# Kernel tuning notes

Measured on AMD Instinct MI355X. Metric: run time of the kernel, lower is better.

Reference implementation:

```python
import jax, jax.numpy as jnp
import numpy as np
from jax import lax

DIM = 64


def _dwconv(x, w, b):
    # x: [B,C,H,W], w: [C,1,kh,kw] depthwise, 'same' padding
    kh, kw = w.shape[2], w.shape[3]
    y = lax.conv_general_dilated(
        x, w, window_strides=(1, 1),
        padding=[(kh // 2, kh // 2), (kw // 2, kw // 2)],
        dimension_numbers=("NCHW", "OIHW", "NCHW"),
        feature_group_count=x.shape[1])
    return y + b[None, :, None, None]


def _conv1x1(x, w, b):
    y = lax.conv_general_dilated(
        x, w, window_strides=(1, 1), padding="VALID",
        dimension_numbers=("NCHW", "OIHW", "NCHW"))
    return y + b[None, :, None, None]


def _avgpool3(x):
    # PyTorch AvgPool2d(3,1,1) default count_include_pad=True -> sum/9
    s = lax.reduce_window(x, 0.0, lax.add, (1, 1, 3, 3), (1, 1, 1, 1),
                          [(0, 0), (0, 0), (1, 1), (1, 1)])
    return s / 9.0


def _maxpool3(x):
    return lax.reduce_window(x, -jnp.inf, lax.max, (1, 1, 3, 3), (1, 1, 1, 1),
                             [(0, 0), (0, 0), (1, 1), (1, 1)])


def setup_inputs() -> dict:
    key = jax.random.key(0)
    ks = jax.random.split(key, 18)
    C = DIM
    def w(k, shape):
        fan_in = shape[1] * shape[2] * shape[3]
        bound = 1.0 / np.sqrt(fan_in)
        return jax.random.uniform(k, shape, jnp.float32, -bound, bound)
    def b(k, fan_in):
        bound = 1.0 / np.sqrt(fan_in)
        return jax.random.uniform(k, (C,), jnp.float32, -bound, bound)
    return {
        "x": jax.random.normal(ks[0], (16, C, 128, 128), jnp.float32),
        "w55": w(ks[1], (C, 1, 5, 5)), "b55": b(ks[2], 25),
        "w17_0": w(ks[3], (C, 1, 1, 7)), "b17_0": b(ks[4], 7),
        "w17_1": w(ks[5], (C, 1, 7, 1)), "b17_1": b(ks[6], 7),
        "w111_0": w(ks[7], (C, 1, 1, 11)), "b111_0": b(ks[8], 11),
        "w111_1": w(ks[9], (C, 1, 11, 1)), "b111_1": b(ks[10], 11),
        "w211_0": w(ks[11], (C, 1, 1, 21)), "b211_0": b(ks[12], 21),
        "w211_1": w(ks[13], (C, 1, 21, 1)), "b211_1": b(ks[14], 21),
        "w11": w(ks[15], (C, C, 1, 1)), "b11": b(ks[16], C),
    }


def reference(x, w55, b55, w17_0, b17_0, w17_1, b17_1,
              w111_0, b111_0, w111_1, b111_1,
              w211_0, b211_0, w211_1, b211_1, w11, b11):
    def branch(inp):
        c55 = _dwconv(inp, w55, b55)
        c17 = _dwconv(_dwconv(inp, w17_0, b17_0), w17_1, b17_1)
        c111 = _dwconv(_dwconv(inp, w111_0, b111_0), w111_1, b111_1)
        c211 = _dwconv(_dwconv(inp, w211_0, b211_0), w211_1, b211_1)
        return _conv1x1(c55 + c17 + c111 + c211, w11, b11)

    mixer = branch(x)
    mixer_1 = branch(_avgpool3(x))
    mixer_2 = branch(_maxpool3(x))
    return (mixer + mixer_1 + mixer_2) * x
```

## Files before the change

### kernel.cpp

```cpp
#include <hip/hip_runtime.h>
#include <hip/hip_bf16.h>
#include <cstdint>

#define HH 128
#define WW 128
#define CC 64
#define BB 16
#define PLANE (HH*WW)
#define TPSTR 16512

#define XS_STR    52
#define XRAW_STR  60
#define XSTH_H    8736
#define H7_H      11328
#define UNION_F   7072
#define H11_H     14144
#define H21_H     16960
#define SMEM_FLOATS 12232

__device__ __forceinline__ float lo16(unsigned int u) {
  return __uint_as_float(u << 16);
}
__device__ __forceinline__ float hi16(unsigned int u) {
  return __uint_as_float(u & 0xffff0000u);
}

__global__ __launch_bounds__(256, 3) void k_dwsum(
    const float* __restrict__ x, float* __restrict__ T,
    const float* __restrict__ w55, const float* __restrict__ b55,
    const float* __restrict__ w17_0, const float* __restrict__ b17_0,
    const float* __restrict__ w17_1, const float* __restrict__ b17_1,
    const float* __restrict__ w111_0, const float* __restrict__ b111_0,
    const float* __restrict__ w111_1, const float* __restrict__ b111_1,
    const float* __restrict__ w211_0, const float* __restrict__ b211_0,
    const float* __restrict__ w211_1, const float* __restrict__ b211_1) {
  __shared__ float sm[SMEM_FLOATS];
  __hip_bfloat16* hb = (__hip_bfloat16*)sm;

  const int bid = blockIdx.x;
  const int pl = bid >> 3;
  const int t = bid & 7;
  const int tR0 = (t >> 2) * 64;
  const int tC0 = (t & 3) * 32;
  const int ch = pl & (CC - 1);
  const float* xp = x + (size_t)pl * PLANE;
  float* Tp = T + (size_t)pl * TPSTR;
  const int tid = threadIdx.x;

  {
    float* xraw = sm + UNION_F;
    const int base_r = tR0 - 11, base_c = tC0 - 12;
    for (int i = tid; i < 86 * 14; i += 256) {
      int rr = i / 14;
      int jj = i - rr * 14;
      int gr = base_r + rr;
      int gc = base_c + jj * 4;
      float4 v = make_float4(0.f, 0.f, 0.f, 0.f);
      if ((unsigned)gr < 128u && (unsigned)gc < 128u)
        v = *(const float4*)(xp + gr * WW + gc);
      *(float4*)(xraw + rr * XRAW_STR + jj * 4) = v;
    }
  }
  __syncthreads();

  {
    const float* xraw = sm + UNION_F;
    __hip_bfloat16* xsTh = hb + XSTH_H;
    for (int i = tid; i < 28 * 13; i += 256) {
      int rg = i % 28;
      int jj = i / 28;
      int rr0 = rg * 3;
      const float* rp = xraw + rr0 * XRAW_STR + jj * 4;
      float w[5][8];
      #pragma unroll
      for (int k = 0; k < 5; ++k) {
        float4 a = *(const float4*)(rp + k * XRAW_STR);
        float4 b = *(const float4*)(rp + k * XRAW_STR + 4);
        w[k][0] = a.x; w[k][1] = a.y; w[k][2] = a.z; w[k][3] = a.w;
        w[k][4] = b.x; w[k][5] = b.y; w[k][6] = b.z; w[k][7] = b.w;
      }
      int gc0 = tC0 + jj * 4 - 12;
      bool cv[7];
      #pragma unroll
      for (int p = 1; p <= 6; ++p) cv[p] = (unsigned)(gc0 + p) < 128u;

      #pragma unroll
      for (int k = 0; k < 3; ++k) {
        int rr = rr0 + k;
        int gr = tR0 + rr - 10;
        bool rv0 = (unsigned)(gr - 1) < 128u;
        bool rv1 = (unsigned)(gr) < 128u;
        bool rv2 = (unsigned)(gr + 1) < 128u;
        float M0[7], M1[7], M2[7];
        #pragma unroll
        for (int p = 1; p <= 6; ++p) {
          M0[p] = (rv0 && cv[p]) ? w[k][p] : -3.402823466e38f;
          M1[p] = (rv1 && cv[p]) ? w[k + 1][p] : -3.402823466e38f;
          M2[p] = (rv2 && cv[p]) ? w[k + 2][p] : -3.402823466e38f;
        }
        float uq[4];
        #pragma unroll
        for (int q = 0; q < 4; ++q) {
          float s = w[k][q + 1] + w[k][q + 2] + w[k][q + 3] + w[k + 1][q + 1] +
                    w[k + 1][q + 2] + w[k + 1][q + 3] + w[k + 2][q + 1] +
                    w[k + 2][q + 2] + w[k + 2][q + 3];
          float m = fmaxf(
              fmaxf(fmaxf(M0[q + 1], M0[q + 2]), fmaxf(M0[q + 3], M1[q + 1])),
              fmaxf(fmaxf(M1[q + 2], M1[q + 3]),
                    fmaxf(fmaxf(M2[q + 1], M2[q + 2]), M2[q + 3])));
          float val = w[k + 1][q + 2] + s * (1.f / 9.f) + m;
          bool vo = rv1 && ((unsigned)(gc0 + q + 2) < 128u);
          uq[q] = vo ? val : 0.f;
        }
        *(float4*)(sm + rr * XS_STR + jj * 4) =
            make_float4(uq[0], uq[1], uq[2], uq[3]);
        int rt = rr - 8;
        if ((unsigned)rt < 68u) {
          #pragma unroll
          for (int q = 0; q < 4; ++q) {
            int ct = jj * 4 + q - 8;
            if ((unsigned)ct < 36u)
              xsTh[ct * 72 + rt] = __float2bfloat16(uq[q]);
          }
        }
      }
    }
  }

  float k7[7], k11[11], k21[21];
  #pragma unroll
  for (int i = 0; i < 7; ++i) k7[i] = w17_0[ch * 7 + i];
  #pragma unroll
  for (int i = 0; i < 11; ++i) k11[i] = w111_0[ch * 11 + i];
  #pragma unroll
  for (int i = 0; i < 21; ++i) k21[i] = w211_0[ch * 21 + i];
  float bb7 = 3.f * b17_0[ch];
  float bb11 = 3.f * b111_0[ch];
  float bb21 = 3.f * b211_0[ch];

  __syncthreads();

  for (int it = tid; it < 84 * 4; it += 256) {
    int rr = it % 84;
    int cg = it / 84;
    float w[28];
    const float* xr = sm + rr * XS_STR + cg * 8;
    #pragma unroll
    for (int j = 0; j < 7; ++j) {
      float4 v = *(const float4*)(xr + 4 * j);
      w[4 * j] = v.x; w[4 * j + 1] = v.y; w[4 * j + 2] = v.z; w[4 * j + 3] = v.w;
    }
    int gr = tR0 + rr - 10;
    bool rv = (unsigned)gr < 128u;
    bool v11r = (rr >= 5) && (rr <= 78);
    bool v7r = (rr >= 7) && (rr <= 76);
    #pragma unroll
    for (int j = 0; j < 8; ++j) {
      float a21 = bb21, a11 = bb11, a7 = bb7;
      #pragma unroll
      for (int d = 0; d < 21; ++d) a21 += k21[d] * w[j + d];
      #pragma unroll
      for (int d = 0; d < 11; ++d) a11 += k11[d] * w[j + 5 + d];
      #pragma unroll
      for (int d = 0; d < 7; ++d) a7 += k7[d] * w[j + 7 + d];
      int c = cg * 8 + j;
      hb[H21_H + c * 88 + rr] = __float2bfloat16(rv ? a21 : 0.f);
      if (v11r) hb[H11_H + c * 88 + rr - 5] = __float2bfloat16(rv ? a11 : 0.f);
      if (v7r) hb[H7_H + c * 88 + rr - 7] = __float2bfloat16(rv ? a7 : 0.f);
    }
  }

  float v7a[7], v11a[11], v21a[21], w5a[25];
  #pragma unroll
  for (int i = 0; i < 7; ++i) v7a[i] = w17_1[ch * 7 + i];
  #pragma unroll
  for (int i = 0; i < 11; ++i) v11a[i] = w111_1[ch * 11 + i];
  #pragma unroll
  for (int i = 0; i < 21; ++i) v21a[i] = w211_1[ch * 21 + i];
  #pragma unroll
  for (int i = 0; i < 25; ++i) w5a[i] = w55[ch * 25 + i];
  float bsum = 3.f * (b55[ch] + b17_1[ch] + b111_1[ch] + b211_1[ch]);

  __syncthreads();

  {
    int c = tid & 31;
    int r0 = (tid >> 5) * 8;
    float acc[8];
    #pragma unroll
    for (int j = 0; j < 8; ++j) acc[j] = bsum;

    float A[28];
    {
      const unsigned* p = (const unsigned*)&hb[H21_H + c * 88 + r0];
      uint4 q0 = *(const uint4*)p;
      uint4 q1 = *(const uint4*)(p + 4);
      uint4 q2 = *(const uint4*)(p + 8);
      uint2 q3 = *(const uint2*)(p + 12);
      A[0]=lo16(q0.x);A[1]=hi16(q0.x);A[2]=lo16(q0.y);A[3]=hi16(q0.y);
      A[4]=lo16(q0.z);A[5]=hi16(q0.z);A[6]=lo16(q0.w);A[7]=hi16(q0.w);
      A[8]=lo16(q1.x);A[9]=hi16(q1.x);A[10]=lo16(q1.y);A[11]=hi16(q1.y);
      A[12]=lo16(q1.z);A[13]=hi16(q1.z);A[14]=lo16(q1.w);A[15]=hi16(q1.w);
      A[16]=lo16(q2.x);A[17]=hi16(q2.x);A[18]=lo16(q2.y);A[19]=hi16(q2.y);
      A[20]=lo16(q2.z);A[21]=hi16(q2.z);A[22]=lo16(q2.w);A[23]=hi16(q2.w);
      A[24]=lo16(q3.x);A[25]=hi16(q3.x);A[26]=lo16(q3.y);A[27]=hi16(q3.y);
      #pragma unroll
      for (int d = 0; d < 21; ++d)
        #pragma unroll
        for (int j = 0; j < 8; ++j) acc[j] += v21a[d] * A[d + j];
    }
    {
      const unsigned* p = (const unsigned*)&hb[H11_H + c * 88 + r0];
      uint4 q0 = *(const uint4*)p;
      uint4 q1 = *(const uint4*)(p + 4);
      uint2 q2 = *(const uint2*)(p + 8);
      A[0]=lo16(q0.x);A[1]=hi16(q0.x);A[2]=lo16(q0.y);A[3]=hi16(q0.y);
      A[4]=lo16(q0.z);A[5]=hi16(q0.z);A[6]=lo16(q0.w);A[7]=hi16(q0.w);
      A[8]=lo16(q1.x);A[9]=hi16(q1.x);A[10]=lo16(q1.y);A[11]=hi16(q1.y);
      A[12]=lo16(q1.z);A[13]=hi16(q1.z);A[14]=lo16(q1.w);A[15]=hi16(q1.w);
      A[16]=lo16(q2.x);A[17]=hi16(q2.x);
      #pragma unroll
      for (int d = 0; d < 11; ++d)
        #pragma unroll
        for (int j = 0; j < 8; ++j) acc[j] += v11a[d] * A[d + j];
    }
    {
      const unsigned* p = (const unsigned*)&hb[H7_H + c * 88 + r0];
      uint4 q0 = *(const uint4*)p;
      uint4 q1 = *(const uint4*)(p + 4);
      A[0]=lo16(q0.x);A[1]=hi16(q0.x);A[2]=lo16(q0.y);A[3]=hi16(q0.y);
      A[4]=lo16(q0.z);A[5]=hi16(q0.z);A[6]=lo16(q0.w);A[7]=hi16(q0.w);
      A[8]=lo16(q1.x);A[9]=hi16(q1.x);A[10]=lo16(q1.y);A[11]=hi16(q1.y);
      A[12]=lo16(q1.z);A[13]=hi16(q1.z);
      #pragma unroll
      for (int d = 0; d < 7; ++d)
        #pragma unroll
        for (int j = 0; j < 8; ++j) acc[j] += v7a[d] * A[d + j];
    }
    {
      #pragma unroll
      for (int dc = 0; dc < 5; ++dc) {
        const unsigned* p = (const unsigned*)&hb[XSTH_H + (c + dc) * 72 + r0];
        uint4 q0 = *(const uint4*)p;
        uint2 q1 = *(const uint2*)(p + 4);
        float X[12];
        X[0]=lo16(q0.x);X[1]=hi16(q0.x);X[2]=lo16(q0.y);X[3]=hi16(q0.y);
        X[4]=lo16(q0.z);X[5]=hi16(q0.z);X[6]=lo16(q0.w);X[7]=hi16(q0.w);
        X[8]=lo16(q1.x);X[9]=hi16(q1.x);X[10]=lo16(q1.y);X[11]=hi16(q1.y);
        #pragma unroll
        for (int dr = 0; dr < 5; ++dr)
          #pragma unroll
          for (int j = 0; j < 8; ++j) acc[j] += w5a[dr * 5 + dc] * X[j + dr];
      }
    }
    #pragma unroll
    for (int j = 0; j < 8; ++j)
      Tp[(size_t)(tR0 + r0 + j) * WW + tC0 + c] = acc[j];
  }
}

__global__ __launch_bounds__(256, 3) void k_mix(const float* __restrict__ T,
                                                const float* __restrict__ x,
                                                const float* __restrict__ w11,
                                                const float* __restrict__ b11,
                                                float* __restrict__ out) {
  __shared__ float sm[64 * 128 + 64 * 68];
  float* Ts = sm;
  float* Wt = sm + 64 * 128;

  int bid = blockIdx.x;
  int b = bid >> 7;
  int px0 = (bid & 127) * 128;
  int tid = threadIdx.x;

  const float* Tb = T + (size_t)b * 64 * TPSTR + px0;
  for (int i = tid; i < 2048; i += 256) {
    int ci = i >> 5;
    int g = (i & 31) * 4;
    *(float4*)(Ts + ci * 128 + g) =
        *(const float4*)(Tb + (size_t)ci * TPSTR + g);
  }
  for (int i = tid; i < 4096; i += 256) {
    int co = i >> 6, ci = i & 63;
    Wt[ci * 68 + co] = w11[i];
  }
  __syncthreads();

  int pxg = tid & 31;
  int cog = tid >> 5;
  const float* tp = Ts + pxg * 4;
  const float* wp = Wt + cog * 8;

  float acc[8][4];
  #pragma unroll
  for (int a = 0; a < 8; ++a)
    #pragma unroll
    for (int p = 0; p < 4; ++p) acc[a][p] = 0.f;

  #pragma unroll
  for (int k = 0; k < 64; ++k) {
    float4 tv = *(const float4*)(tp + k * 128);
    float4 q0 = *(const float4*)(wp + k * 68);
    float4 q1 = *(const float4*)(wp + k * 68 + 4);
    float wf[8] = {q0.x, q0.y, q0.z, q0.w, q1.x, q1.y, q1.z, q1.w};
    float tvv[4] = {tv.x, tv.y, tv.z, tv.w};
    #pragma unroll
    for (int a = 0; a < 8; ++a)
      #pragma unroll
      for (int p = 0; p < 4; ++p) acc[a][p] += wf[a] * tvv[p];
  }

  const float* xb = x + (size_t)b * (CC * PLANE) + px0 + pxg * 4;
  float* ob = out + (size_t)b * (CC * PLANE) + px0 + pxg * 4;
  #pragma unroll
  for (int a = 0; a < 8; ++a) {
    int co = cog * 8 + a;
    float bb = 3.f * b11[co];
    float4 xv = *(const float4*)(xb + (size_t)co * PLANE);
    float4 o;
    o.x = (acc[a][0] + bb) * xv.x;
    o.y = (acc[a][1] + bb) * xv.y;
    o.z = (acc[a][2] + bb) * xv.z;
    o.w = (acc[a][3] + bb) * xv.w;
    *(float4*)(ob + (size_t)co * PLANE) = o;
  }
}

extern "C" void kernel_launch(void* const* d_in, const int* in_sizes, int n_in,
                              void* d_out, int out_size, void* d_ws,
                              size_t ws_size, hipStream_t stream) {
  const float* x = (const float*)d_in[0];
  const float* w55 = (const float*)d_in[1];
  const float* b55 = (const float*)d_in[2];
  const float* w17_0 = (const float*)d_in[3];
  const float* b17_0 = (const float*)d_in[4];
  const float* w17_1 = (const float*)d_in[5];
  const float* b17_1 = (const float*)d_in[6];
  const float* w111_0 = (const float*)d_in[7];
  const float* b111_0 = (const float*)d_in[8];
  const float* w111_1 = (const float*)d_in[9];
  const float* b111_1 = (const float*)d_in[10];
  const float* w211_0 = (const float*)d_in[11];
  const float* b211_0 = (const float*)d_in[12];
  const float* w211_1 = (const float*)d_in[13];
  const float* b211_1 = (const float*)d_in[14];
  const float* w11 = (const float*)d_in[15];
  const float* b11 = (const float*)d_in[16];
  float* outp = (float*)d_out;

  float* T = (float*)d_ws;

  k_dwsum<<<BB * CC * 8, 256, 0, stream>>>(
      x, T, w55, b55, w17_0, b17_0, w17_1, b17_1, w111_0, b111_0, w111_1,
      b111_1, w211_0, b211_0, w211_1, b211_1);
  k_mix<<<BB * 128, 256, 0, stream>>>(T, x, w11, b11, outp);
}
```

Before: 306.2 us.

## Halve dwsum raw staging buffer and double-buffer mix kernel with direct LDS loads

k_dwsum now loads the input halo tile in two 44-row halves into a smaller raw buffer, running the pool/transpose phase per half. This cuts shared memory so launch bounds can rise to 4 blocks per CU, at the cost of an extra barrier round. k_mix now streams T in 16-channel chunks into a double-buffered LDS tile using global_load_lds, and prefetches x early. Both aim to overlap loads with FMA work and raise occupancy, but they add synchronisation and extra register pressure from holding the x values.

```diff
diff --git a/kernel.cpp b/kernel.cpp
--- a/kernel.cpp
+++ b/kernel.cpp
@@ -16,7 +16,7 @@
 #define UNION_F   7072
 #define H11_H     14144
 #define H21_H     16960
-#define SMEM_FLOATS 12232
+#define SMEM_FLOATS 9888
 
 __device__ __forceinline__ float lo16(unsigned int u) {
   return __uint_as_float(u << 16);
@@ -25,7 +25,72 @@
   return __uint_as_float(u & 0xffff0000u);
 }
 
-__global__ __launch_bounds__(256, 3) void k_dwsum(
+__device__ __forceinline__ void phase_a2_half(
+    float* sm, __hip_bfloat16* hb, const float* xbuf, int tid, int tR0,
+    int tC0, int rg_lo, int roff) {
+  __hip_bfloat16* xsTh = hb + XSTH_H;
+  for (int i = tid; i < 14 * 13; i += 256) {
+    int rg = rg_lo + (i % 14);
+    int jj = i / 14;
+    int rr0 = rg * 3;
+    const float* rp = xbuf + (rr0 - roff) * XRAW_STR + jj * 4;
+    float w[5][8];
+    #pragma unroll
+    for (int k = 0; k < 5; ++k) {
+      float4 a = *(const float4*)(rp + k * XRAW_STR);
+      float4 b = *(const float4*)(rp + k * XRAW_STR + 4);
+      w[k][0] = a.x; w[k][1] = a.y; w[k][2] = a.z; w[k][3] = a.w;
+      w[k][4] = b.x; w[k][5] = b.y; w[k][6] = b.z; w[k][7] = b.w;
+    }
+    int gc0 = tC0 + jj * 4 - 12;
+    bool cv[7];
+    #pragma unroll
+    for (int p = 1; p <= 6; ++p) cv[p] = (unsigned)(gc0 + p) < 128u;
+
+    #pragma unroll
+    for (int k = 0; k < 3; ++k) {
+      int rr = rr0 + k;
+      int gr = tR0 + rr - 10;
+      bool rv0 = (unsigned)(gr - 1) < 128u;
+      bool rv1 = (unsigned)(gr) < 128u;
+      bool rv2 = (unsigned)(gr + 1) < 128u;
+      float M0[7], M1[7], M2[7];
+      #pragma unroll
+      for (int p = 1; p <= 6; ++p) {
+        M0[p] = (rv0 && cv[p]) ? w[k][p] : -3.402823466e38f;
+        M1[p] = (rv1 && cv[p]) ? w[k + 1][p] : -3.402823466e38f;
+        M2[p] = (rv2 && cv[p]) ? w[k + 2][p] : -3.402823466e38f;
+      }
+      float uq[4];
+      #pragma unroll
+      for (int q = 0; q < 4; ++q) {
+        float s = w[k][q + 1] + w[k][q + 2] + w[k][q + 3] + w[k + 1][q + 1] +
+                  w[k + 1][q + 2] + w[k + 1][q + 3] + w[k + 2][q + 1] +
+                  w[k + 2][q + 2] + w[k + 2][q + 3];
+        float m = fmaxf(
+            fmaxf(fmaxf(M0[q + 1], M0[q + 2]), fmaxf(M0[q + 3], M1[q + 1])),
+            fmaxf(fmaxf(M1[q + 2], M1[q + 3]),
+                  fmaxf(fmaxf(M2[q + 1], M2[q + 2]), M2[q + 3])));
+        float val = w[k + 1][q + 2] + s * (1.f / 9.f) + m;
+        bool vo = rv1 && ((unsigned)(gc0 + q + 2) < 128u);
+        uq[q] = vo ? val : 0.f;
+      }
+      *(float4*)(sm + rr * XS_STR + jj * 4) =
+          make_float4(uq[0], uq[1], uq[2], uq[3]);
+      int rt = rr - 8;
+      if ((unsigned)rt < 68u) {
+        #pragma unroll
+        for (int q = 0; q < 4; ++q) {
+          int ct = jj * 4 + q - 8;
+          if ((unsigned)ct < 36u)
+            xsTh[ct * 72 + rt] = __float2bfloat16(uq[q]);
+        }
+      }
+    }
+  }
+}
+
+__global__ __launch_bounds__(256, 4) void k_dwsum(
     const float* __restrict__ x, float* __restrict__ T,
     const float* __restrict__ w55, const float* __restrict__ b55,
     const float* __restrict__ w17_0, const float* __restrict__ b17_0,
@@ -47,85 +112,34 @@
   float* Tp = T + (size_t)pl * TPSTR;
   const int tid = threadIdx.x;
 
-  {
-    float* xraw = sm + UNION_F;
-    const int base_r = tR0 - 11, base_c = tC0 - 12;
-    for (int i = tid; i < 86 * 14; i += 256) {
-      int rr = i / 14;
-      int jj = i - rr * 14;
-      int gr = base_r + rr;
-      int gc = base_c + jj * 4;
-      float4 v = make_float4(0.f, 0.f, 0.f, 0.f);
-      if ((unsigned)gr < 128u && (unsigned)gc < 128u)
-        v = *(const float4*)(xp + gr * WW + gc);
-      *(float4*)(xraw + rr * XRAW_STR + jj * 4) = v;
-    }
-  }
-  __syncthreads();
-
-  {
-    const float* xraw = sm + UNION_F;
-    __hip_bfloat16* xsTh = hb + XSTH_H;
-    for (int i = tid; i < 28 * 13; i += 256) {
-      int rg = i % 28;
-      int jj = i / 28;
-      int rr0 = rg * 3;
-      const float* rp = xraw + rr0 * XRAW_STR + jj * 4;
-      float w[5][8];
-      #pragma unroll
-      for (int k = 0; k < 5; ++k) {
-        float4 a = *(const float4*)(rp + k * XRAW_STR);
-        float4 b = *(const float4*)(rp + k * XRAW_STR + 4);
-        w[k][0] = a.x; w[k][1] = a.y; w[k][2] = a.z; w[k][3] = a.w;
-        w[k][4] = b.x; w[k][5] = b.y; w[k][6] = b.z; w[k][7] = b.w;
-      }
-      int gc0 = tC0 + jj * 4 - 12;
-      bool cv[7];
-      #pragma unroll
-      for (int p = 1; p <= 6; ++p) cv[p] = (unsigned)(gc0 + p) < 128u;
-
-      #pragma unroll
-      for (int k = 0; k < 3; ++k) {
-        int rr = rr0 + k;
-        int gr = tR0 + rr - 10;
-        bool rv0 = (unsigned)(gr - 1) < 128u;
-        bool rv1 = (unsigned)(gr) < 128u;
-        bool rv2 = (unsigned)(gr + 1) < 128u;
-        float M0[7], M1[7], M2[7];
-        #pragma unroll
-        for (int p = 1; p <= 6; ++p) {
-          M0[p] = (rv0 && cv[p]) ? w[k][p] : -3.402823466e38f;
-          M1[p] = (rv1 && cv[p]) ? w[k + 1][p] : -3.402823466e38f;
-          M2[p] = (rv2 && cv[p]) ? w[k + 2][p] : -3.402823466e38f;
-        }
-        float uq[4];
-        #pragma unroll
-        for (int q = 0; q < 4; ++q) {
-          float s = w[k][q + 1] + w[k][q + 2] + w[k][q + 3] + w[k + 1][q + 1] +
-                    w[k + 1][q + 2] + w[k + 1][q + 3] + w[k + 2][q + 1] +
-                    w[k + 2][q + 2] + w[k + 2][q + 3];
-          float m = fmaxf(
-              fmaxf(fmaxf(M0[q + 1], M0[q + 2]), fmaxf(M0[q + 3], M1[q + 1])),
-              fmaxf(fmaxf(M1[q + 2], M1[q + 3]),
-                    fmaxf(fmaxf(M2[q + 1], M2[q + 2]), M2[q + 3])));
-          float val = w[k + 1][q + 2] + s * (1.f / 9.f) + m;
-          bool vo = rv1 && ((unsigned)(gc0 + q + 2) < 128u);
-          uq[q] = vo ? val : 0.f;
-        }
-        *(float4*)(sm + rr * XS_STR + jj * 4) =
-            make_float4(uq[0], uq[1], uq[2], uq[3]);
-        int rt = rr - 8;
-        if ((unsigned)rt < 68u) {
-          #pragma unroll
-          for (int q = 0; q < 4; ++q) {
-            int ct = jj * 4 + q - 8;
-            if ((unsigned)ct < 36u)
-              xsTh[ct * 72 + rt] = __float2bfloat16(uq[q]);
-          }
-        }
-      }
-    }
-  }
+  float* xbuf = sm + UNION_F;
+  const int base_r = tR0 - 11, base_c = tC0 - 12;
+
+  for (int i = tid; i < 44 * 14; i += 256) {
+    int rr = i / 14;
+    int jj = i - rr * 14;
+    int gr = base_r + rr;
+    int gc = base_c + jj * 4;
+    float4 v = make_float4(0.f, 0.f, 0.f, 0.f);
+    if ((unsigned)gr < 128u && (unsigned)gc < 128u)
+      v = *(const float4*)(xp + gr * WW + gc);
+    *(float4*)(xbuf + rr * XRAW_STR + jj * 4) = v;
+  }
+  __syncthreads();
+  phase_a2_half(sm, hb, xbuf, tid, tR0, tC0, 0, 0);
+  __syncthreads();
+  for (int i = tid; i < 44 * 14; i += 256) {
+    int rr = i / 14;
+    int jj = i - rr * 14;
+    int gr = base_r + 42 + rr;
+    int gc = base_c + jj * 4;
+    float4 v = make_float4(0.f, 0.f, 0.f, 0.f);
+    if ((unsigned)gr < 128u && (unsigned)gc < 128u)
+      v = *(const float4*)(xp + gr * WW + gc);
+    *(float4*)(xbuf + rr * XRAW_STR + jj * 4) = v;
+  }
+  __syncthreads();
+  phase_a2_half(sm, hb, xbuf, tid, tR0, tC0, 14, 42);
 
   float k7[7], k11[11], k21[21];
   #pragma unroll
@@ -259,69 +273,92 @@
   }
 }
 
-__global__ __launch_bounds__(256, 3) void k_mix(const float* __restrict__ T,
+__device__ __forceinline__ void gload_lds16(const float* g, float* l) {
+  __builtin_amdgcn_global_load_lds(
+      (const __attribute__((address_space(1))) void*)g,
+      (__attribute__((address_space(3))) void*)l, 16, 0, 0);
+}
+
+__global__ __launch_bounds__(256, 4) void k_mix(const float* __restrict__ T,
                                                 const float* __restrict__ x,
                                                 const float* __restrict__ w11,
                                                 const float* __restrict__ b11,
                                                 float* __restrict__ out) {
-  __shared__ float sm[64 * 128 + 64 * 68];
-  float* Ts = sm;
-  float* Wt = sm + 64 * 128;
+  __shared__ float Tbuf[2][16 * 128];
+  __shared__ float Wt[64 * 68];
 
   int bid = blockIdx.x;
   int b = bid >> 7;
   int px0 = (bid & 127) * 128;
   int tid = threadIdx.x;
+  int lane = tid & 63;
+  int wv = tid >> 6;
 
   const float* Tb = T + (size_t)b * 64 * TPSTR + px0;
-  for (int i = tid; i < 2048; i += 256) {
-    int ci = i >> 5;
-    int g = (i & 31) * 4;
-    *(float4*)(Ts + ci * 128 + g) =
-        *(const float4*)(Tb + (size_t)ci * TPSTR + g);
-  }
+
+  const int srow = wv * 4 + (lane >> 5);
+  const int scol = (lane & 31) * 4;
+
+  #pragma unroll
+  for (int j = 0; j < 2; ++j)
+    gload_lds16(Tb + (size_t)(srow + j * 2) * TPSTR + scol,
+                &Tbuf[0][(wv * 4 + j * 2) * 128]);
+
   for (int i = tid; i < 4096; i += 256) {
     int co = i >> 6, ci = i & 63;
     Wt[ci * 68 + co] = w11[i];
   }
-  __syncthreads();
 
   int pxg = tid & 31;
   int cog = tid >> 5;
-  const float* tp = Ts + pxg * 4;
   const float* wp = Wt + cog * 8;
 
+  const float* xb = x + (size_t)b * (CC * PLANE) + px0 + pxg * 4;
+  float4 xv[8];
+  #pragma unroll
+  for (int a = 0; a < 8; ++a)
+    xv[a] = *(const float4*)(xb + (size_t)(cog * 8 + a) * PLANE);
+
   float acc[8][4];
   #pragma unroll
   for (int a = 0; a < 8; ++a)
     #pragma unroll
     for (int p = 0; p < 4; ++p) acc[a][p] = 0.f;
 
-  #pragma unroll
-  for (int k = 0; k < 64; ++k) {
-    float4 tv = *(const float4*)(tp + k * 128);
-    float4 q0 = *(const float4*)(wp + k * 68);
-    float4 q1 = *(const float4*)(wp + k * 68 + 4);
-    float wf[8] = {q0.x, q0.y, q0.z, q0.w, q1.x, q1.y, q1.z, q1.w};
-    float tvv[4] = {tv.x, tv.y, tv.z, tv.w};
-    #pragma unroll
-    for (int a = 0; a < 8; ++a)
-      #pragma unroll
-      for (int p = 0; p < 4; ++p) acc[a][p] += wf[a] * tvv[p];
-  }
-
-  const float* xb = x + (size_t)b * (CC * PLANE) + px0 + pxg * 4;
+  for (int q = 0; q < 4; ++q) {
+    __syncthreads();
+    if (q < 3) {
+      #pragma unroll
+      for (int j = 0; j < 2; ++j)
+        gload_lds16(Tb + (size_t)((q + 1) * 16 + srow + j * 2) * TPSTR + scol,
+                    &Tbuf[(q + 1) & 1][(wv * 4 + j * 2) * 128]);
+    }
+    const float* tp = Tbuf[q & 1] + pxg * 4;
+    #pragma unroll
+    for (int kk = 0; kk < 16; ++kk) {
+      int k = q * 16 + kk;
+      float4 tv = *(const float4*)(tp + kk * 128);
+      float4 q0 = *(const float4*)(wp + k * 68);
+      float4 q1 = *(const float4*)(wp + k * 68 + 4);
+      float wf[8] = {q0.x, q0.y, q0.z, q0.w, q1.x, q1.y, q1.z, q1.w};
+      float tvv[4] = {tv.x, tv.y, tv.z, tv.w};
+      #pragma unroll
+      for (int a = 0; a < 8; ++a)
+        #pragma unroll
+        for (int p = 0; p < 4; ++p) acc[a][p] += wf[a] * tvv[p];
+    }
+  }
+
   float* ob = out + (size_t)b * (CC * PLANE) + px0 + pxg * 4;
   #pragma unroll
   for (int a = 0; a < 8; ++a) {
     int co = cog * 8 + a;
     float bb = 3.f * b11[co];
-    float4 xv = *(const float4*)(xb + (size_t)co * PLANE);
     float4 o;
-    o.x = (acc[a][0] + bb) * xv.x;
-    o.y = (acc[a][1] + bb) * xv.y;
-    o.z = (acc[a][2] + bb) * xv.z;
-    o.w = (acc[a][3] + bb) * xv.w;
+    o.x = (acc[a][0] + bb) * xv[a].x;
+    o.y = (acc[a][1] + bb) * xv[a].y;
+    o.z = (acc[a][2] + bb) * xv[a].z;
+    o.w = (acc[a][3] + bb) * xv[a].w;
     *(float4*)(ob + (size_t)co * PLANE) = o;
   }
 }
```

After: 307.1 us. About the same (+0.3%).
